# Kernel optimization log

Hardware: AMD Instinct MI355X
Metric: run time of the kernel (lower is better)

Reference implementation:

```python
import jax, jax.numpy as jnp
import numpy as np

C_IN = 256
C_RED = max(4, C_IN // 4)  # 64


def setup_inputs() -> dict:
    key = jax.random.key(0)
    k1, k2, k3, k4, k5 = jax.random.split(key, 5)
    B, C, H, W = 4, C_IN, 64, 64
    x = jax.random.normal(k1, (B, C, H, W), dtype=jnp.float32)
    # 1x1 convs (no bias) are just channel matmuls: weight shape (out_ch, in_ch)
    s_in = 1.0 / np.sqrt(C)
    s_red = 1.0 / np.sqrt(C_RED)
    Wq = jax.random.normal(k2, (C_RED, C), dtype=jnp.float32) * s_in
    Wk = jax.random.normal(k3, (C_RED, C), dtype=jnp.float32) * s_in
    Wv = jax.random.normal(k4, (C_RED, C), dtype=jnp.float32) * s_in
    Wp = jax.random.normal(k5, (C, C_RED), dtype=jnp.float32) * s_red
    return {"x": x, "Wq": Wq, "Wk": Wk, "Wv": Wv, "Wp": Wp}


def reference(x, Wq, Wk, Wv, Wp):
    B, C, H, W = x.shape
    N = H * W
    xf = x.reshape(B, C, N)                       # (B, C, N)
    q = jnp.einsum('rc,bcn->bnr', Wq, xf)         # (B, N, c_red)
    k = jnp.einsum('rc,bcn->brn', Wk, xf)         # (B, c_red, N)
    v = jnp.einsum('rc,bcn->bnr', Wv, xf)         # (B, N, c_red)
    scale = 1.0 / jnp.sqrt(jnp.float32(k.shape[1]))
    attn = jnp.einsum('bnr,brm->bnm', q, k) * scale   # (B, N, N)
    attn = jax.nn.softmax(attn, axis=-1)
    out = jnp.einsum('bnm,bmr->brn', attn, v)     # (B, c_red, N)
    out = jnp.einsum('cr,brn->bcn', Wp, out)      # (B, C, N)
    return out.reshape(B, C, H, W) + x
```

## Files before the change

### kernel.cpp

```cpp
#include <hip/hip_runtime.h>
#include <hip/hip_bf16.h>

#define CIN 256
#define CRED 64
#define NB 4
#define NN 4096

typedef float v4f __attribute__((ext_vector_type(4)));
typedef short v8s __attribute__((ext_vector_type(8)));
typedef unsigned short u16;
typedef u16 u16x4 __attribute__((ext_vector_type(4)));
typedef u16 u16x8 __attribute__((ext_vector_type(8)));
typedef unsigned int u32;

#define LOG2E 1.4426950408889634f

__device__ __forceinline__ u16 f2bf(float f) {
    union { float f; u32 u; } v; v.f = f;
    u32 r = (v.u + 0x7FFFu + ((v.u >> 16) & 1u)) >> 16;
    return (u16)r;
}
__device__ __forceinline__ float bf2f(u16 s) {
    union { u32 u; float f; } v; v.u = ((u32)s) << 16;
    return v.f;
}
__device__ __forceinline__ u32 pkbf(float a, float b) {
    float2 f; f.x = a; f.y = b;
    __hip_bfloat162 h = __float22bfloat162_rn(f);
    union { __hip_bfloat162 h; u32 u; } c; c.h = h;
    return c.u;
}
__device__ __forceinline__ v4f mfma16(v8s a, v8s b, v4f c) {
    return __builtin_amdgcn_mfma_f32_16x16x32_bf16(a, b, c, 0, 0, 0);
}
__device__ __forceinline__ float fexp2(float x) {
#if __has_builtin(__builtin_amdgcn_exp2f)
    return __builtin_amdgcn_exp2f(x);
#else
    return exp2f(x);
#endif
}

__global__ __launch_bounds__(256) void k_wconv(const float* __restrict__ Wq,
                                               const float* __restrict__ Wk,
                                               const float* __restrict__ Wv,
                                               const float* __restrict__ Wp,
                                               u16* __restrict__ Wb,
                                               u16* __restrict__ WpB) {
    int t = threadIdx.x;
    if (blockIdx.x < 48) {
        int idx = (blockIdx.x * 256 + t) * 4;
        int row = idx >> 8;
        int mat = row >> 6, r = row & 63, col = idx & 255;
        const float* src = (mat == 0) ? Wq : (mat == 1) ? Wk : Wv;
        float4 v = *(const float4*)&src[r * 256 + col];
        float s = (mat == 0) ? (0.125f * LOG2E) : 1.0f;
        u16x4 o;
        o[0] = f2bf(v.x * s); o[1] = f2bf(v.y * s);
        o[2] = f2bf(v.z * s); o[3] = f2bf(v.w * s);
        *(u16x4*)&Wb[idx] = o;
    } else {
        int idx = ((blockIdx.x - 48) * 256 + t) * 4;
        float4 v = *(const float4*)&Wp[idx];
        u16x4 o;
        o[0] = f2bf(v.x); o[1] = f2bf(v.y);
        o[2] = f2bf(v.z); o[3] = f2bf(v.w);
        *(u16x4*)&WpB[idx] = o;
    }
}

__global__ __launch_bounds__(256) void k_qkvm(const float* __restrict__ x,
                                              const u16* __restrict__ Wb,
                                              u16* __restrict__ Q, u16* __restrict__ K,
                                              u16* __restrict__ V) {
    int t = threadIdx.x;
    int wv = t >> 6, lane = t & 63, c15 = lane & 15, quad = lane >> 4;
    int n0g = blockIdx.x * 32;
    int b = n0g >> 12, nb = n0g & 4095;
    const float* xb = x + ((size_t)b << 20);

    v8s Af[2][8];
#pragma unroll
    for (int nt = 0; nt < 2; ++nt) {
        const float* px = xb + nb + nt * 16 + c15 + (size_t)quad * 8 * 4096;
#pragma unroll
        for (int kc = 0; kc < 8; ++kc) {
            float f[8];
#pragma unroll
            for (int j = 0; j < 8; ++j)
                f[j] = px[((size_t)kc * 32 + j) * 4096];
            union { v8s s; u32 w[4]; } pk;
            pk.w[0] = pkbf(f[0], f[1]); pk.w[1] = pkbf(f[2], f[3]);
            pk.w[2] = pkbf(f[4], f[5]); pk.w[3] = pkbf(f[6], f[7]);
            Af[nt][kc] = pk.s;
        }
    }

#pragma unroll
    for (int rti = 0; rti < 3; ++rti) {
        int rt = wv * 3 + rti;
        const u16* wrow = Wb + (size_t)(rt * 16 + c15) * 256 + quad * 8;
        v8s Bf[8];
#pragma unroll
        for (int kc = 0; kc < 8; ++kc) Bf[kc] = *(const v8s*)&wrow[kc * 32];
#pragma unroll
        for (int nt = 0; nt < 2; ++nt) {
            v4f acc = {0.f, 0.f, 0.f, 0.f};
#pragma unroll
            for (int kc = 0; kc < 8; ++kc)
                acc = mfma16(Af[nt][kc], Bf[kc], acc);
            if (rt < 8) {
                u16* base = (rt < 4) ? Q : K;
                u16* dst = base + ((size_t)b << 18)
                         + (size_t)(nb + nt * 16 + quad * 4) * 64
                         + (rt & 3) * 16 + c15;
#pragma unroll
                for (int g = 0; g < 4; ++g) dst[g * 64] = f2bf(acc[g]);
            } else {
                int hi2 = ((nb + nt * 16) >> 4) & 3;
                size_t base = ((size_t)b * 64 + (rt - 8) * 16 + c15) * 4096
                            + (size_t)((nb + nt * 16) & ~63) + hi2;
#pragma unroll
                for (int g = 0; g < 4; ++g)
                    V[base + (quad * 4 + g) * 4] = f2bf(acc[g]);
            }
        }
    }
}

__global__ __launch_bounds__(256, 4) void k_flash(const u16* __restrict__ Q,
                                                  const u16* __restrict__ K,
                                                  const u16* __restrict__ V,
                                                  u16* __restrict__ OP,
                                                  float* __restrict__ Lb,
                                                  int sh) {
    __shared__ u16 Kl[64][72];
    __shared__ u16 Vl[64][72];
    __shared__ u16 Pl[4][32][72];
    int t = threadIdx.x;
    int p = blockIdx.x & ((1u << sh) - 1);
    int tile = blockIdx.x >> sh;
    int b = tile >> 5;
    int n0 = (tile & 31) * 128;
    int wv = t >> 6;
    int lane = t & 63;
    int c15 = lane & 15;
    int quad = lane >> 4;
    int nw = n0 + wv * 32;
    const u16* Qb = Q + (size_t)b * NN * 64;
    const u16* Kb = K + (size_t)b * NN * 64;
    const u16* Vb = V + (size_t)b * 64 * NN;

    v8s Qa[2][2];
#pragma unroll
    for (int rg = 0; rg < 2; ++rg)
#pragma unroll
        for (int c2 = 0; c2 < 2; ++c2)
            Qa[rg][c2] = *(const v8s*)&Qb[(size_t)(nw + rg * 16 + c15) * 64 + c2 * 32 + quad * 8];

    v4f O[2][4];
    float ls[2][4];
#pragma unroll
    for (int rg = 0; rg < 2; ++rg)
#pragma unroll
        for (int g = 0; g < 4; ++g) {
            ls[rg][g] = 0.f;
#pragma unroll
            for (int cg = 0; cg < 4; ++cg) O[rg][cg][g] = 0.f;
        }

    int mlen = NN >> sh;
    int m0 = p * mlen;
    int iters = mlen >> 6;
    for (int it = 0; it < iters; ++it) {
        int mt = m0 + it * 64;
        int srow = t >> 3, scol = (t & 7) * 8;
#pragma unroll
        for (int pass = 0; pass < 2; ++pass) {
            int rr = srow + pass * 32;
            *(v8s*)&Kl[rr][scol] = *(const v8s*)&Kb[(size_t)(mt + rr) * 64 + scol];
            *(v8s*)&Vl[rr][scol] = *(const v8s*)&Vb[(size_t)rr * NN + mt + scol];
        }
        __syncthreads();

        v4f S[2][4];
#pragma unroll
        for (int rg = 0; rg < 2; ++rg)
#pragma unroll
            for (int s = 0; s < 4; ++s)
#pragma unroll
                for (int g = 0; g < 4; ++g) S[rg][s][g] = 0.f;
#pragma unroll
        for (int s = 0; s < 4; ++s)
#pragma unroll
            for (int c2 = 0; c2 < 2; ++c2) {
                v8s kb = *(const v8s*)&Kl[s * 16 + c15][c2 * 32 + quad * 8];
                S[0][s] = mfma16(Qa[0][c2], kb, S[0][s]);
                S[1][s] = mfma16(Qa[1][c2], kb, S[1][s]);
            }

#pragma unroll
        for (int rg = 0; rg < 2; ++rg) {
            float E[4][4];
#pragma unroll
            for (int s = 0; s < 4; ++s)
#pragma unroll
                for (int g = 0; g < 4; ++g) {
                    float e = fexp2(S[rg][s][g]);
                    E[s][g] = e;
                    ls[rg][g] += e;
                }
#pragma unroll
            for (int g = 0; g < 4; ++g) {
                union { u16x4 v; u32 w[2]; } p2;
                p2.w[0] = pkbf(E[0][g], E[1][g]);
                p2.w[1] = pkbf(E[2][g], E[3][g]);
                *(u16x4*)&Pl[wv][rg * 16 + quad * 4 + g][c15 * 4] = p2.v;
            }
        }

        v8s Pa[2][2];
#pragma unroll
        for (int rg = 0; rg < 2; ++rg)
#pragma unroll
            for (int c2 = 0; c2 < 2; ++c2)
                Pa[rg][c2] = *(const v8s*)&Pl[wv][rg * 16 + c15][c2 * 32 + quad * 8];
#pragma unroll
        for (int cg = 0; cg < 4; ++cg)
#pragma unroll
            for (int c2 = 0; c2 < 2; ++c2) {
                v8s vb = *(const v8s*)&Vl[cg * 16 + c15][c2 * 32 + quad * 8];
                O[0][cg] = mfma16(Pa[0][c2], vb, O[0][cg]);
                O[1][cg] = mfma16(Pa[1][c2], vb, O[1][cg]);
            }
        __syncthreads();
    }

    u16* OPp = OP + (size_t)p * (NB * NN * 64) + (size_t)b * NN * 64;
#pragma unroll
    for (int rg = 0; rg < 2; ++rg)
#pragma unroll
        for (int cg = 0; cg < 4; ++cg)
#pragma unroll
            for (int g = 0; g < 4; ++g) {
                int n = nw + rg * 16 + quad * 4 + g;
                OPp[(size_t)n * 64 + cg * 16 + c15] = f2bf(O[rg][cg][g]);
            }
#pragma unroll
    for (int rg = 0; rg < 2; ++rg)
#pragma unroll
        for (int g = 0; g < 4; ++g) {
            float v = ls[rg][g];
#pragma unroll
            for (int off = 1; off <= 8; off <<= 1) v += __shfl_xor(v, off);
            ls[rg][g] = v;
        }
    if (c15 == 0) {
        float* Lp = Lb + (size_t)p * (NB * NN) + (size_t)b * NN;
#pragma unroll
        for (int rg = 0; rg < 2; ++rg)
#pragma unroll
            for (int g = 0; g < 4; ++g) {
                int n = nw + rg * 16 + quad * 4 + g;
                Lp[n] = ls[rg][g];
            }
    }
}

#define OMP 72
__global__ __launch_bounds__(256) void k_proj(const u16* __restrict__ OP,
                                              const float* __restrict__ Lb,
                                              const u16* __restrict__ WpB,
                                              const float* __restrict__ x,
                                              float* __restrict__ out,
                                              int nsp) {
    __shared__ u16 Om[16 * OMP];
    int t = threadIdx.x;
    int b = blockIdx.x >> 8;
    int n0 = (blockIdx.x & 255) * 16;

    {
        int n_l = t >> 4, r0 = (t & 15) * 4;
        size_t nidx = (size_t)b * NN + n0 + n_l;
        float o[4] = {0.f, 0.f, 0.f, 0.f};
        float l = 0.f;
        for (int p = 0; p < nsp; ++p) {
            u16x4 u = *(const u16x4*)&OP[((size_t)p * (NB * NN) + nidx) * 64 + r0];
#pragma unroll
            for (int j = 0; j < 4; ++j) o[j] += bf2f(u[j]);
            l += Lb[(size_t)p * (NB * NN) + nidx];
        }
        float inv = 1.0f / l;
        union { u16x4 v; u32 w[2]; } p2;
        p2.w[0] = pkbf(o[0] * inv, o[1] * inv);
        p2.w[1] = pkbf(o[2] * inv, o[3] * inv);
        *(u16x4*)&Om[n_l * OMP + r0] = p2.v;
    }
    __syncthreads();

    int lane = t & 63, wvv = t >> 6, c15 = lane & 15, quad = lane >> 4;
    v8s B0 = *(const v8s*)&Om[c15 * OMP + quad * 8];
    v8s B1 = *(const v8s*)&Om[c15 * OMP + 32 + quad * 8];
#pragma unroll
    for (int ct0 = 0; ct0 < 4; ++ct0) {
        int ct = wvv * 4 + ct0;
        const u16* wrow = WpB + (size_t)(ct * 16 + c15) * 64 + quad * 8;
        v8s A0 = *(const v8s*)&wrow[0];
        v8s A1 = *(const v8s*)&wrow[32];
        v4f acc = {0.f, 0.f, 0.f, 0.f};
        acc = mfma16(A0, B0, acc);
        acc = mfma16(A1, B1, acc);
        size_t base = ((size_t)(b * 256 + ct * 16 + quad * 4)) * 4096 + n0 + c15;
#pragma unroll
        for (int g = 0; g < 4; ++g)
            out[base + (size_t)g * 4096] = acc[g] + x[base + (size_t)g * 4096];
    }
}

extern "C" void kernel_launch(void* const* d_in, const int* in_sizes, int n_in,
                              void* d_out, int out_size, void* d_ws, size_t ws_size,
                              hipStream_t stream) {
    const float* x  = (const float*)d_in[0];
    const float* Wq = (const float*)d_in[1];
    const float* Wk = (const float*)d_in[2];
    const float* Wv = (const float*)d_in[3];
    const float* Wp = (const float*)d_in[4];
    float* out = (float*)d_out;
    char* ws = (char*)d_ws;

    int nsp = (ws_size >= (size_t)24 * 1024 * 1024) ? 8 : 4;
    int sh = (nsp == 8) ? 3 : 2;

    u16* Wb  = (u16*)(ws);
    u16* WpB = (u16*)(ws + 131072);
    u16* Q   = (u16*)(ws + 262144);
    u16* K   = (u16*)(ws + 262144 + 2097152);
    u16* V   = (u16*)(ws + 262144 + 2 * 2097152);
    u16* OP  = (u16*)(ws + 262144 + 3 * 2097152);
    float* Lbuf = (float*)(ws + 262144 + (size_t)(3 + nsp) * 2097152);

    k_wconv<<<64, 256, 0, stream>>>(Wq, Wk, Wv, Wp, Wb, WpB);
    k_qkvm<<<512, 256, 0, stream>>>(x, Wb, Q, K, V);
    k_flash<<<NB * 32 * nsp, 256, 0, stream>>>(Q, K, V, OP, Lbuf, sh);
    k_proj<<<NB * 256, 256, 0, stream>>>(OP, Lbuf, WpB, x, out, nsp);
}
```

Measured before the change: 126.5 us.

## Load K/V fragments directly from global in flash kernel, halve qkv tile

The flash attention kernel no longer stages K and V tiles in shared memory with block barriers. Each wave now loads its MFMA operand fragments straight from global memory through the caches. This removes LDS writes, LDS reads and two __syncthreads per iteration, at the cost of four waves redundantly fetching the same K/V data. The QKV projection kernel is also split into smaller 16-column tiles with twice as many blocks, and weight fragments are loaded per k-chunk.

```diff
diff --git a/kernel.cpp b/kernel.cpp
--- a/kernel.cpp
+++ b/kernel.cpp
@@ -75,14 +75,13 @@
                                               u16* __restrict__ V) {
     int t = threadIdx.x;
     int wv = t >> 6, lane = t & 63, c15 = lane & 15, quad = lane >> 4;
-    int n0g = blockIdx.x * 32;
-    int b = n0g >> 12, nb = n0g & 4095;
+    int b = blockIdx.x >> 8;
+    int nb = (blockIdx.x & 255) * 16;
     const float* xb = x + ((size_t)b << 20);
 
-    v8s Af[2][8];
-#pragma unroll
-    for (int nt = 0; nt < 2; ++nt) {
-        const float* px = xb + nb + nt * 16 + c15 + (size_t)quad * 8 * 4096;
+    v8s Af[8];
+    {
+        const float* px = xb + nb + c15 + (size_t)quad * 8 * 4096;
 #pragma unroll
         for (int kc = 0; kc < 8; ++kc) {
             float f[8];
@@ -92,7 +91,7 @@
             union { v8s s; u32 w[4]; } pk;
             pk.w[0] = pkbf(f[0], f[1]); pk.w[1] = pkbf(f[2], f[3]);
             pk.w[2] = pkbf(f[4], f[5]); pk.w[3] = pkbf(f[6], f[7]);
-            Af[nt][kc] = pk.s;
+            Af[kc] = pk.s;
         }
     }
 
@@ -100,30 +99,25 @@
     for (int rti = 0; rti < 3; ++rti) {
         int rt = wv * 3 + rti;
         const u16* wrow = Wb + (size_t)(rt * 16 + c15) * 256 + quad * 8;
-        v8s Bf[8];
-#pragma unroll
-        for (int kc = 0; kc < 8; ++kc) Bf[kc] = *(const v8s*)&wrow[kc * 32];
-#pragma unroll
-        for (int nt = 0; nt < 2; ++nt) {
-            v4f acc = {0.f, 0.f, 0.f, 0.f};
-#pragma unroll
-            for (int kc = 0; kc < 8; ++kc)
-                acc = mfma16(Af[nt][kc], Bf[kc], acc);
-            if (rt < 8) {
-                u16* base = (rt < 4) ? Q : K;
-                u16* dst = base + ((size_t)b << 18)
-                         + (size_t)(nb + nt * 16 + quad * 4) * 64
-                         + (rt & 3) * 16 + c15;
-#pragma unroll
-                for (int g = 0; g < 4; ++g) dst[g * 64] = f2bf(acc[g]);
-            } else {
-                int hi2 = ((nb + nt * 16) >> 4) & 3;
-                size_t base = ((size_t)b * 64 + (rt - 8) * 16 + c15) * 4096
-                            + (size_t)((nb + nt * 16) & ~63) + hi2;
-#pragma unroll
-                for (int g = 0; g < 4; ++g)
-                    V[base + (quad * 4 + g) * 4] = f2bf(acc[g]);
-            }
+        v4f acc = {0.f, 0.f, 0.f, 0.f};
+#pragma unroll
+        for (int kc = 0; kc < 8; ++kc) {
+            v8s Bf = *(const v8s*)&wrow[kc * 32];
+            acc = mfma16(Af[kc], Bf, acc);
+        }
+        if (rt < 8) {
+            u16* base = (rt < 4) ? Q : K;
+            u16* dst = base + ((size_t)b << 18)
+                     + (size_t)(nb + quad * 4) * 64 + (rt & 3) * 16 + c15;
+#pragma unroll
+            for (int g = 0; g < 4; ++g) dst[g * 64] = f2bf(acc[g]);
+        } else {
+            int hi2 = (nb >> 4) & 3;
+            size_t base = ((size_t)b * 64 + (rt - 8) * 16 + c15) * 4096
+                        + (size_t)(nb & ~63) + hi2;
+#pragma unroll
+            for (int g = 0; g < 4; ++g)
+                V[base + (quad * 4 + g) * 4] = f2bf(acc[g]);
         }
     }
 }
@@ -134,8 +128,6 @@
                                                   u16* __restrict__ OP,
                                                   float* __restrict__ Lb,
                                                   int sh) {
-    __shared__ u16 Kl[64][72];
-    __shared__ u16 Vl[64][72];
     __shared__ u16 Pl[4][32][72];
     int t = threadIdx.x;
     int p = blockIdx.x & ((1u << sh) - 1);
@@ -148,40 +140,34 @@
     int quad = lane >> 4;
     int nw = n0 + wv * 32;
     const u16* Qb = Q + (size_t)b * NN * 64;
-    const u16* Kb = K + (size_t)b * NN * 64;
-    const u16* Vb = V + (size_t)b * 64 * NN;
-
-    v8s Qa[2][2];
-#pragma unroll
-    for (int rg = 0; rg < 2; ++rg)
-#pragma unroll
-        for (int c2 = 0; c2 < 2; ++c2)
-            Qa[rg][c2] = *(const v8s*)&Qb[(size_t)(nw + rg * 16 + c15) * 64 + c2 * 32 + quad * 8];
-
-    v4f O[2][4];
-    float ls[2][4];
-#pragma unroll
-    for (int rg = 0; rg < 2; ++rg)
-#pragma unroll
-        for (int g = 0; g < 4; ++g) {
-            ls[rg][g] = 0.f;
-#pragma unroll
-            for (int cg = 0; cg < 4; ++cg) O[rg][cg][g] = 0.f;
-        }
-
     int mlen = NN >> sh;
     int m0 = p * mlen;
     int iters = mlen >> 6;
+
+    const u16* kp = K + (size_t)b * NN * 64 + (size_t)(m0 + c15) * 64 + quad * 8;
+    const u16* vp = V + (size_t)b * 64 * NN + (size_t)c15 * NN + m0 + quad * 8;
+
+    v8s Qa[2][2];
+#pragma unroll
+    for (int rg = 0; rg < 2; ++rg)
+#pragma unroll
+        for (int c2 = 0; c2 < 2; ++c2)
+            Qa[rg][c2] = *(const v8s*)&Qb[(size_t)(nw + rg * 16 + c15) * 64 + c2 * 32 + quad * 8];
+
+    v4f O[2][4];
+    float ls[2][4];
+#pragma unroll
+    for (int rg = 0; rg < 2; ++rg)
+#pragma unroll
+        for (int g = 0; g < 4; ++g) {
+            ls[rg][g] = 0.f;
+#pragma unroll
+            for (int cg = 0; cg < 4; ++cg) O[rg][cg][g] = 0.f;
+        }
+
     for (int it = 0; it < iters; ++it) {
-        int mt = m0 + it * 64;
-        int srow = t >> 3, scol = (t & 7) * 8;
-#pragma unroll
-        for (int pass = 0; pass < 2; ++pass) {
-            int rr = srow + pass * 32;
-            *(v8s*)&Kl[rr][scol] = *(const v8s*)&Kb[(size_t)(mt + rr) * 64 + scol];
-            *(v8s*)&Vl[rr][scol] = *(const v8s*)&Vb[(size_t)rr * NN + mt + scol];
-        }
-        __syncthreads();
+        size_t ko = (size_t)it * 64 * 64;
+        size_t vo = (size_t)it * 64;
 
         v4f S[2][4];
 #pragma unroll
@@ -191,13 +177,14 @@
 #pragma unroll
                 for (int g = 0; g < 4; ++g) S[rg][s][g] = 0.f;
 #pragma unroll
-        for (int s = 0; s < 4; ++s)
-#pragma unroll
-            for (int c2 = 0; c2 < 2; ++c2) {
-                v8s kb = *(const v8s*)&Kl[s * 16 + c15][c2 * 32 + quad * 8];
-                S[0][s] = mfma16(Qa[0][c2], kb, S[0][s]);
-                S[1][s] = mfma16(Qa[1][c2], kb, S[1][s]);
-            }
+        for (int s = 0; s < 4; ++s) {
+            v8s kb0 = *(const v8s*)&kp[ko + (size_t)s * 16 * 64];
+            v8s kb1 = *(const v8s*)&kp[ko + (size_t)s * 16 * 64 + 32];
+            S[0][s] = mfma16(Qa[0][0], kb0, S[0][s]);
+            S[1][s] = mfma16(Qa[1][0], kb0, S[1][s]);
+            S[0][s] = mfma16(Qa[0][1], kb1, S[0][s]);
+            S[1][s] = mfma16(Qa[1][1], kb1, S[1][s]);
+        }
 
 #pragma unroll
         for (int rg = 0; rg < 2; ++rg) {
@@ -226,14 +213,14 @@
             for (int c2 = 0; c2 < 2; ++c2)
                 Pa[rg][c2] = *(const v8s*)&Pl[wv][rg * 16 + c15][c2 * 32 + quad * 8];
 #pragma unroll
-        for (int cg = 0; cg < 4; ++cg)
-#pragma unroll
-            for (int c2 = 0; c2 < 2; ++c2) {
-                v8s vb = *(const v8s*)&Vl[cg * 16 + c15][c2 * 32 + quad * 8];
-                O[0][cg] = mfma16(Pa[0][c2], vb, O[0][cg]);
-                O[1][cg] = mfma16(Pa[1][c2], vb, O[1][cg]);
-            }
-        __syncthreads();
+        for (int cg = 0; cg < 4; ++cg) {
+            v8s vb0 = *(const v8s*)&vp[(size_t)cg * 16 * NN + vo];
+            v8s vb1 = *(const v8s*)&vp[(size_t)cg * 16 * NN + vo + 32];
+            O[0][cg] = mfma16(Pa[0][0], vb0, O[0][cg]);
+            O[1][cg] = mfma16(Pa[1][0], vb0, O[1][cg]);
+            O[0][cg] = mfma16(Pa[0][1], vb1, O[0][cg]);
+            O[1][cg] = mfma16(Pa[1][1], vb1, O[1][cg]);
+        }
     }
 
     u16* OPp = OP + (size_t)p * (NB * NN * 64) + (size_t)b * NN * 64;
@@ -340,7 +327,7 @@
     float* Lbuf = (float*)(ws + 262144 + (size_t)(3 + nsp) * 2097152);
 
     k_wconv<<<64, 256, 0, stream>>>(Wq, Wk, Wv, Wp, Wb, WpB);
-    k_qkvm<<<512, 256, 0, stream>>>(x, Wb, Q, K, V);
+    k_qkvm<<<NB * 256, 256, 0, stream>>>(x, Wb, Q, K, V);
     k_flash<<<NB * 32 * nsp, 256, 0, stream>>>(Q, K, V, OP, Lbuf, sh);
     k_proj<<<NB * 256, 256, 0, stream>>>(OP, Lbuf, WpB, x, out, nsp);
 }
```

Measured after the change: 168.7 us. 1.33x slower.
